# Optimization experiments

Hardware: AMD Instinct MI355X
Metric: run time of the kernel (lower is better)

The kernel has to match this reference:

```python
import jax, jax.numpy as jnp
import numpy as np

B, S, D = 2, 2048, 1280
H = 20
HD = D // H  # 64, rotary dim


def setup_inputs() -> dict:
    key = jax.random.key(0)
    ks = jax.random.split(key, 4)
    scale = 0.02
    return {
        "hidden_states": jax.random.normal(ks[0], (B, S, D), jnp.float32),
        "Wq": jax.random.normal(ks[1], (D, D), jnp.float32) * scale,
        "bq": jnp.zeros((D,), jnp.float32),
        "Wk": jax.random.normal(ks[2], (D, D), jnp.float32) * scale,
        "bk": jnp.zeros((D,), jnp.float32),
        "Wv": jax.random.normal(ks[3], (D, D), jnp.float32) * scale,
        "bv": jnp.zeros((D,), jnp.float32),
    }


def _rotate_half(x):
    x1, x2 = jnp.split(x, 2, axis=-1)
    return jnp.concatenate((-x2, x1), axis=-1)


def _rotary_cos_sin(seq_len, dim, dtype):
    inv_freq = 1.0 / (10000.0 ** (jnp.arange(0, dim, 2, dtype=jnp.float32) / dim))
    t = jnp.arange(seq_len, dtype=jnp.float32)
    freqs = jnp.einsum("i,j->ij", t, inv_freq)          # [S, dim/2]
    emb = jnp.concatenate((freqs, freqs), axis=-1)        # [S, dim]
    return jnp.cos(emb).astype(dtype)[None, None], jnp.sin(emb).astype(dtype)[None, None]


def reference(hidden_states, Wq, bq, Wk, bk, Wv, bv):
    b, s, d = hidden_states.shape
    # QKV projections, split heads -> [B, H, S, HD]
    def proj(W, bias):
        y = hidden_states @ W + bias
        return y.reshape(b, s, H, HD).transpose(0, 2, 1, 3)

    q = proj(Wq, bq) * (HD ** -0.5)  # scale BEFORE rotary, as in source
    k = proj(Wk, bk)
    v = proj(Wv, bv)

    cos, sin = _rotary_cos_sin(s, HD, q.dtype)
    q = q * cos + _rotate_half(q) * sin
    k = k * cos + _rotate_half(k) * sin

    scores = jnp.einsum("bhqd,bhkd->bhqk", q, k)
    probs = jax.nn.softmax(scores, axis=-1)
    ctx = jnp.einsum("bhqk,bhkd->bhqd", probs, v)
    return ctx.transpose(0, 2, 1, 3).reshape(b, s, d)
```

## Files before the change

### kernel.cpp

```cpp
#include <hip/hip_runtime.h>

#define DD 1280
#define SS 2048
#define HH 20

typedef __bf16 bf16x8 __attribute__((ext_vector_type(8)));
typedef float f32x4 __attribute__((ext_vector_type(4)));

typedef __attribute__((address_space(3))) unsigned int lds_uint;
typedef __attribute__((address_space(1))) unsigned int glb_uint;
#define GLL16(g, l) __builtin_amdgcn_global_load_lds((const glb_uint*)(g), (lds_uint*)(l), 16, 0, 0)

__device__ __forceinline__ unsigned short f2bf(float f) {
  union { float f; unsigned u; } v; v.f = f;
  unsigned r = v.u + 0x7fffu + ((v.u >> 16) & 1u);
  return (unsigned short)(r >> 16);
}
__device__ __forceinline__ unsigned f2u(float f) {
  union { float f; unsigned u; } v; v.f = f; return v.u;
}
__device__ __forceinline__ unsigned pk2(float lo, float hi) {
  return ((unsigned)f2bf(hi) << 16) | (unsigned)f2bf(lo);
}

__global__ __launch_bounds__(256) void prep_kernel(
    const float* __restrict__ X, const float* __restrict__ Wq,
    const float* __restrict__ Wk, const float* __restrict__ Wv,
    unsigned short* __restrict__ Xb, unsigned short* __restrict__ WT,
    float2* __restrict__ cs) {
  __shared__ __align__(8) unsigned short tile[32][36];
  int bid = blockIdx.x, tid = threadIdx.x;
  if (bid < 2560) {
    size_t base = (size_t)bid * 2048 + (size_t)tid * 8;
    const float4* xin = (const float4*)(X + base);
    float4 a = xin[0], c = xin[1];
    uint4 o = make_uint4(pk2(a.x, a.y), pk2(a.z, a.w), pk2(c.x, c.y), pk2(c.z, c.w));
    *(uint4*)(Xb + base) = o;
  } else if (bid < 7360) {
    int wb = bid - 2560;
    int mat = wb / 1600;
    int t = wb % 1600;
    int tn = t % 40, tk = t / 40;
    const float* W = (mat == 0) ? Wq : ((mat == 1) ? Wk : Wv);
    int k0 = tk * 32, n0 = tn * 32;
    int r = tid >> 3, cq = tid & 7;
    float4 wv = *(const float4*)(W + (size_t)(k0 + r) * DD + n0 + cq * 4);
    *(ushort4*)&tile[r][cq * 4] =
        make_ushort4(f2bf(wv.x), f2bf(wv.y), f2bf(wv.z), f2bf(wv.w));
    __syncthreads();
    unsigned short* out = WT + (size_t)mat * DD * DD;
    ushort4 o = make_ushort4(tile[cq * 4 + 0][r], tile[cq * 4 + 1][r],
                             tile[cq * 4 + 2][r], tile[cq * 4 + 3][r]);
    *(ushort4*)(out + (size_t)(n0 + r) * DD + k0 + cq * 4) = o;
  } else {
    int idx = (bid - 7360) * 256 + tid;
    int sp = idx >> 5, j = idx & 31;
    float invf = exp2f(-(float)j * 0.41524101186092034f);
    float ang = (float)sp * invf;
    cs[idx] = make_float2(cosf(ang), sinf(ang));
  }
}

__global__ __launch_bounds__(256) void qkv_gemm_kernel(
    const unsigned short* __restrict__ Xb, const unsigned short* __restrict__ WT,
    const float* __restrict__ bq, const float* __restrict__ bk, const float* __restrict__ bv,
    const float2* __restrict__ cs,
    unsigned short* __restrict__ Qr, unsigned short* __restrict__ Kr,
    unsigned short* __restrict__ VT) {
  __shared__ __align__(16) unsigned short As[128 * 32];
  __shared__ __align__(16) unsigned short Bs[128 * 32];
  int bx0 = blockIdx.x;
  int bx = (bx0 & 7) * 120 + (bx0 >> 3);
  int mat = bx / 320;
  int r0 = bx % 320;
  int tm = r0 / 10, tn = r0 % 10;
  int m0 = tm * 128, n0 = tn * 128;
  int tid = threadIdx.x;
  int lane = tid & 63, wave = tid >> 6;
  int c15 = lane & 15, quad = lane >> 4;
  int wm = wave >> 1, wn = wave & 1;
  const unsigned short* Wm = WT + (size_t)mat * DD * DD;

  int rowA = tid >> 2;
  int c8 = (tid & 3) * 8;
  const unsigned short* gA0 = Xb + (size_t)(m0 + rowA) * DD + c8;
  const unsigned short* gA1 = gA0 + (size_t)64 * DD;
  const unsigned short* gB0 = Wm + (size_t)(n0 + rowA) * DD + c8;
  const unsigned short* gB1 = gB0 + (size_t)64 * DD;
  unsigned short* ldsA0 = As + wave * 512;
  unsigned short* ldsA1 = As + 2048 + wave * 512;
  unsigned short* ldsB0 = Bs + wave * 512;
  unsigned short* ldsB1 = Bs + 2048 + wave * 512;

  f32x4 acc[4][4] = {};

  for (int kk = 0; kk < DD; kk += 32) {
    __syncthreads();
    GLL16(gA0 + kk, ldsA0);
    GLL16(gA1 + kk, ldsA1);
    GLL16(gB0 + kk, ldsB0);
    GLL16(gB1 + kk, ldsB1);
    __syncthreads();
    bf16x8 af[4];
#pragma unroll
    for (int mi = 0; mi < 4; mi++)
      af[mi] = *(const bf16x8*)(As + (wm * 64 + mi * 16 + c15) * 32 + quad * 8);
#pragma unroll
    for (int ni = 0; ni < 4; ni++) {
      bf16x8 bfr = *(const bf16x8*)(Bs + (wn * 64 + ni * 16 + c15) * 32 + quad * 8);
#pragma unroll
      for (int mi = 0; mi < 4; mi++)
        acc[mi][ni] = __builtin_amdgcn_mfma_f32_16x16x32_bf16(af[mi], bfr, acc[mi][ni], 0, 0, 0);
    }
  }

  int growb = m0 + wm * 64;
  int gcolb = n0 + wn * 64;
  if (mat == 2) {
#pragma unroll
    for (int mi = 0; mi < 4; mi++) {
      int row0 = growb + mi * 16 + quad * 4;
      int bb_ = row0 >> 11, sp = row0 & 2047;
#pragma unroll
      for (int ni = 0; ni < 4; ni++) {
        int gcol = gcolb + ni * 16 + c15;
        float bias = bv[gcol];
        int hh = gcol >> 6, dd = gcol & 63;
        f32x4 v = acc[mi][ni];
        ushort4 o = make_ushort4(f2bf(v[0] + bias), f2bf(v[1] + bias),
                                 f2bf(v[2] + bias), f2bf(v[3] + bias));
        *(ushort4*)(VT + ((size_t)((bb_ * HH + hh) * 64 + dd)) * SS + sp) = o;
      }
    }
  } else {
    unsigned short* Out = (mat == 0) ? Qr : Kr;
    const float* bias = (mat == 0) ? bq : bk;
    float qs = (mat == 0) ? 0.18033688011112042f : 1.0f;
#pragma unroll
    for (int mi = 0; mi < 4; mi++) {
      int row0 = growb + mi * 16 + quad * 4;
#pragma unroll
      for (int ni = 0; ni < 2; ni++) {
        int gcol_lo = gcolb + ni * 16 + c15;
        int gcol_hi = gcol_lo + 32;
        float blo = bias[gcol_lo], bhi = bias[gcol_hi];
        int d = ni * 16 + c15;
        f32x4 lo = acc[mi][ni], hi = acc[mi][ni + 2];
#pragma unroll
        for (int r = 0; r < 4; r++) {
          int grow = row0 + r;
          float2 cv = cs[(size_t)(grow & 2047) * 32 + d];
          float xl = (lo[r] + blo) * qs, xh = (hi[r] + bhi) * qs;
          Out[(size_t)grow * DD + gcol_lo] = f2bf(xl * cv.x - xh * cv.y);
          Out[(size_t)grow * DD + gcol_hi] = f2bf(xh * cv.x + xl * cv.y);
        }
      }
    }
  }
}

__device__ __forceinline__ void attn_load_frags(
    bf16x8 (&kf)[2][2], bf16x8 (&vf)[4],
    const unsigned short* Kt, const unsigned short* Vt, int c15, int quad) {
#pragma unroll
  for (int ni = 0; ni < 2; ni++)
#pragma unroll
    for (int kc = 0; kc < 2; kc++)
      kf[ni][kc] = *(const bf16x8*)(Kt + (size_t)(ni * 16 + c15) * DD + kc * 32 + quad * 8);
#pragma unroll
  for (int nio = 0; nio < 4; nio++)
    vf[nio] = *(const bf16x8*)(Vt + (size_t)(nio * 16 + c15) * SS + quad * 8);
}

__device__ __forceinline__ void attn_tile(
    const bf16x8 (&qf)[4][2], const bf16x8 (&kf)[2][2], const bf16x8 (&vf)[4],
    const bf16x8& ones, f32x4 (&of)[4][4], f32x4 (&ol)[4],
    unsigned short* Pw, int c15, int quad) {
  f32x4 sc[4][2] = {};
#pragma unroll
  for (int ni = 0; ni < 2; ni++)
#pragma unroll
    for (int kc = 0; kc < 2; kc++)
#pragma unroll
      for (int mi = 0; mi < 4; mi++)
        sc[mi][ni] = __builtin_amdgcn_mfma_f32_16x16x32_bf16(qf[mi][kc], kf[ni][kc], sc[mi][ni], 0, 0, 0);

  int pos_r = (quad + 2 * ((c15 >> 2) & 3) + (c15 & 3)) & 7;

#define PROD(mi)                                                              \
  {                                                                           \
    _Pragma("unroll")                                                         \
    for (int ni = 0; ni < 2; ni++) {                                          \
      int kc8 = ni * 2 + (c15 >> 3);                                          \
      _Pragma("unroll")                                                       \
      for (int r = 0; r < 4; r++) {                                           \
        unsigned u = f2u(__builtin_amdgcn_exp2f(sc[mi][ni][r]));              \
        int q = (mi) * 16 + quad * 4 + r;                                     \
        int pos = (kc8 + 2 * quad + r) & 7;                                   \
        Pw[q * 64 + pos * 8 + (c15 & 7)] = (unsigned short)(u >> 16);         \
      }                                                                       \
    }                                                                         \
  }
#define CONS(mi)                                                              \
  {                                                                           \
    bf16x8 pf = *(const bf16x8*)(Pw + ((mi) * 16 + c15) * 64 + pos_r * 8);    \
    _Pragma("unroll")                                                         \
    for (int nio = 0; nio < 4; nio++)                                         \
      of[mi][nio] = __builtin_amdgcn_mfma_f32_16x16x32_bf16(pf, vf[nio],      \
                                                            of[mi][nio], 0, 0, 0); \
    ol[mi] = __builtin_amdgcn_mfma_f32_16x16x32_bf16(pf, ones, ol[mi], 0, 0, 0); \
  }

  PROD(0);
  PROD(1); CONS(0);
  PROD(2); CONS(1);
  PROD(3); CONS(2);
  CONS(3);
#undef PROD
#undef CONS
}

__global__ __launch_bounds__(256)
__attribute__((amdgpu_waves_per_eu(2, 4)))
void attn_kernel(
    const unsigned short* __restrict__ Qr, const unsigned short* __restrict__ Kr,
    const unsigned short* __restrict__ VT, float* __restrict__ out) {
  __shared__ __align__(16) unsigned short Pall[4 * 64 * 64];
  __shared__ float Lbuf[64];
  int bx = blockIdx.x;
  int bh = bx % 40, qt = bx / 40;
  int b = bh / HH, h = bh % HH;
  int tid = threadIdx.x;
  int lane = tid & 63, w = tid >> 6;
  int c15 = lane & 15, quad = lane >> 4;
  int q0 = qt * 64;

  const unsigned short* Qbase = Qr + (size_t)(b * SS + q0) * DD + h * 64;
  bf16x8 qf[4][2];
#pragma unroll
  for (int mi = 0; mi < 4; mi++)
#pragma unroll
    for (int kc = 0; kc < 2; kc++)
      qf[mi][kc] = *(const bf16x8*)(Qbase + (size_t)(mi * 16 + c15) * DD + kc * 32 + quad * 8);

  const unsigned short* Kbase = Kr + (size_t)(b * SS + w * 32) * DD + h * 64;
  const unsigned short* Vbase = VT + (size_t)(bh * 64) * SS + w * 32;
  unsigned short* Pw = Pall + w * 4096;

  bf16x8 ones;
#pragma unroll
  for (int i = 0; i < 8; i++) ones[i] = (__bf16)1.0f;

  f32x4 of[4][4] = {};
  f32x4 ol[4] = {};

  bf16x8 kfb[2][2][2], vfb[2][4];
  attn_load_frags(kfb[0], vfb[0], Kbase, Vbase, c15, quad);

  for (int t = 0; t < 16; t += 2) {
    attn_load_frags(kfb[1], vfb[1],
                    Kbase + (size_t)((t + 1) * 128) * DD, Vbase + (t + 1) * 128,
                    c15, quad);
    attn_tile(qf, kfb[0], vfb[0], ones, of, ol, Pw, c15, quad);
    if (t + 2 < 16)
      attn_load_frags(kfb[0], vfb[0],
                      Kbase + (size_t)((t + 2) * 128) * DD, Vbase + (t + 2) * 128,
                      c15, quad);
    attn_tile(qf, kfb[1], vfb[1], ones, of, ol, Pw, c15, quad);
  }

  __syncthreads();
  float* Obuf = (float*)Pall;

  for (int pass = 0; pass < 4; pass++) {
    if (w == pass) {
#pragma unroll
      for (int mi = 0; mi < 4; mi++)
#pragma unroll
        for (int nio = 0; nio < 4; nio++)
#pragma unroll
          for (int r = 0; r < 4; r++) {
            int q = mi * 16 + quad * 4 + r;
            int d = nio * 16 + c15;
            if (pass == 0) Obuf[q * 65 + d] = of[mi][nio][r];
            else           Obuf[q * 65 + d] += of[mi][nio][r];
          }
      if (c15 == 0) {
#pragma unroll
        for (int mi = 0; mi < 4; mi++)
#pragma unroll
          for (int r = 0; r < 4; r++) {
            int q = mi * 16 + quad * 4 + r;
            if (pass == 0) Lbuf[q] = ol[mi][r];
            else           Lbuf[q] += ol[mi][r];
          }
      }
    }
    __syncthreads();
  }

  {
    int row = w * 16 + (lane >> 2);
    int col0 = (lane & 3) * 16;
    float invl = 1.0f / Lbuf[row];
    float* op = out + (size_t)(b * SS + q0 + row) * DD + h * 64 + col0;
    const float* ob = Obuf + row * 65 + col0;
#pragma unroll
    for (int j = 0; j < 4; j++) {
      float4 v = make_float4(ob[j * 4 + 0] * invl, ob[j * 4 + 1] * invl,
                             ob[j * 4 + 2] * invl, ob[j * 4 + 3] * invl);
      *(float4*)(op + j * 4) = v;
    }
  }
}

extern "C" void kernel_launch(void* const* d_in, const int* in_sizes, int n_in,
                              void* d_out, int out_size, void* d_ws, size_t ws_size,
                              hipStream_t stream) {
  (void)in_sizes; (void)n_in; (void)out_size; (void)ws_size;
  const float* X  = (const float*)d_in[0];
  const float* Wq = (const float*)d_in[1];
  const float* bq = (const float*)d_in[2];
  const float* Wk = (const float*)d_in[3];
  const float* bk = (const float*)d_in[4];
  const float* Wv = (const float*)d_in[5];
  const float* bv = (const float*)d_in[6];
  char* ws = (char*)d_ws;
  unsigned short* Xb  = (unsigned short*)(ws);
  unsigned short* WT  = (unsigned short*)(ws + 10485760);
  unsigned short* Qr  = (unsigned short*)(ws + 20316160);
  unsigned short* Kr  = (unsigned short*)(ws + 30801920);
  unsigned short* VTt = (unsigned short*)(ws + 41287680);
  float2* cstab       = (float2*)(ws + 51773440);
  hipLaunchKernelGGL(prep_kernel, dim3(7616), dim3(256), 0, stream, X, Wq, Wk, Wv, Xb, WT, cstab);
  hipLaunchKernelGGL(qkv_gemm_kernel, dim3(960), dim3(256), 0, stream, Xb, WT, bq, bk, bv, cstab, Qr, Kr, VTt);
  hipLaunchKernelGGL(attn_kernel, dim3(1280), dim3(256), 0, stream, Qr, Kr, VTt, (float*)d_out);
}
```

Baseline: 242.2 us.

## Restructure attention to split queries across waves with shared LDS K/V tiles

The attention kernel now gives each wave its own 16 query rows instead of having all four waves split the key range over the same 64 queries. K and V tiles of 32 keys are staged once per block into double-buffered, XOR-swizzled LDS with global_load_lds, and all waves share them. This removes the cross-wave reduction of partial outputs and row sums through LDS at the end, and cuts register use. The cost is a block-wide barrier on every one of the 64 key steps and smaller MFMA work per step, which may expose latency. The waves_per_eu attribute is also dropped.

New measurement: 234.0 us. 1.04x faster.

```diff
diff --git a/kernel.cpp b/kernel.cpp
--- a/kernel.cpp
+++ b/kernel.cpp
@@ -159,158 +159,93 @@
   }
 }
 
-__device__ __forceinline__ void attn_load_frags(
-    bf16x8 (&kf)[2][2], bf16x8 (&vf)[4],
-    const unsigned short* Kt, const unsigned short* Vt, int c15, int quad) {
-#pragma unroll
-  for (int ni = 0; ni < 2; ni++)
-#pragma unroll
-    for (int kc = 0; kc < 2; kc++)
-      kf[ni][kc] = *(const bf16x8*)(Kt + (size_t)(ni * 16 + c15) * DD + kc * 32 + quad * 8);
-#pragma unroll
-  for (int nio = 0; nio < 4; nio++)
-    vf[nio] = *(const bf16x8*)(Vt + (size_t)(nio * 16 + c15) * SS + quad * 8);
-}
-
-__device__ __forceinline__ void attn_tile(
-    const bf16x8 (&qf)[4][2], const bf16x8 (&kf)[2][2], const bf16x8 (&vf)[4],
-    const bf16x8& ones, f32x4 (&of)[4][4], f32x4 (&ol)[4],
-    unsigned short* Pw, int c15, int quad) {
-  f32x4 sc[4][2] = {};
-#pragma unroll
-  for (int ni = 0; ni < 2; ni++)
-#pragma unroll
-    for (int kc = 0; kc < 2; kc++)
-#pragma unroll
-      for (int mi = 0; mi < 4; mi++)
-        sc[mi][ni] = __builtin_amdgcn_mfma_f32_16x16x32_bf16(qf[mi][kc], kf[ni][kc], sc[mi][ni], 0, 0, 0);
-
-  int pos_r = (quad + 2 * ((c15 >> 2) & 3) + (c15 & 3)) & 7;
-
-#define PROD(mi)                                                              \
-  {                                                                           \
-    _Pragma("unroll")                                                         \
-    for (int ni = 0; ni < 2; ni++) {                                          \
-      int kc8 = ni * 2 + (c15 >> 3);                                          \
-      _Pragma("unroll")                                                       \
-      for (int r = 0; r < 4; r++) {                                           \
-        unsigned u = f2u(__builtin_amdgcn_exp2f(sc[mi][ni][r]));              \
-        int q = (mi) * 16 + quad * 4 + r;                                     \
-        int pos = (kc8 + 2 * quad + r) & 7;                                   \
-        Pw[q * 64 + pos * 8 + (c15 & 7)] = (unsigned short)(u >> 16);         \
-      }                                                                       \
-    }                                                                         \
-  }
-#define CONS(mi)                                                              \
-  {                                                                           \
-    bf16x8 pf = *(const bf16x8*)(Pw + ((mi) * 16 + c15) * 64 + pos_r * 8);    \
-    _Pragma("unroll")                                                         \
-    for (int nio = 0; nio < 4; nio++)                                         \
-      of[mi][nio] = __builtin_amdgcn_mfma_f32_16x16x32_bf16(pf, vf[nio],      \
-                                                            of[mi][nio], 0, 0, 0); \
-    ol[mi] = __builtin_amdgcn_mfma_f32_16x16x32_bf16(pf, ones, ol[mi], 0, 0, 0); \
-  }
-
-  PROD(0);
-  PROD(1); CONS(0);
-  PROD(2); CONS(1);
-  PROD(3); CONS(2);
-  CONS(3);
-#undef PROD
-#undef CONS
-}
-
 __global__ __launch_bounds__(256)
-__attribute__((amdgpu_waves_per_eu(2, 4)))
 void attn_kernel(
     const unsigned short* __restrict__ Qr, const unsigned short* __restrict__ Kr,
     const unsigned short* __restrict__ VT, float* __restrict__ out) {
-  __shared__ __align__(16) unsigned short Pall[4 * 64 * 64];
-  __shared__ float Lbuf[64];
+  __shared__ __align__(16) unsigned short Klds[2][2048];
+  __shared__ __align__(16) unsigned short Vlds[2][2048];
+  __shared__ __align__(16) unsigned short Pall[4][512];
   int bx = blockIdx.x;
   int bh = bx % 40, qt = bx / 40;
   int b = bh / HH, h = bh % HH;
   int tid = threadIdx.x;
   int lane = tid & 63, w = tid >> 6;
   int c15 = lane & 15, quad = lane >> 4;
-  int q0 = qt * 64;
-
-  const unsigned short* Qbase = Qr + (size_t)(b * SS + q0) * DD + h * 64;
-  bf16x8 qf[4][2];
-#pragma unroll
-  for (int mi = 0; mi < 4; mi++)
+  int q0 = qt * 64 + w * 16;
+
+  const unsigned short* Qb = Qr + (size_t)(b * SS + q0 + c15) * DD + h * 64 + quad * 8;
+  bf16x8 qf[2];
+  qf[0] = *(const bf16x8*)(Qb);
+  qf[1] = *(const bf16x8*)(Qb + 32);
+
+  int krow = tid >> 3, kch = tid & 7;
+  const unsigned short* Ksrc = Kr + (size_t)(b * SS + krow) * DD + h * 64
+                               + ((kch ^ (krow & 7)) * 8);
+  int vrow = tid >> 2, vch = tid & 3;
+  const unsigned short* Vsrc = VT + (size_t)(bh * 64 + vrow) * SS
+                               + ((vch ^ ((vrow >> 1) & 3)) * 8);
+  unsigned short* Pw = &Pall[w][0];
+
+  bf16x8 ones;
+#pragma unroll
+  for (int i = 0; i < 8; i++) ones[i] = (__bf16)1.0f;
+
+  f32x4 of[4] = {};
+  f32x4 ol = {};
+
+  GLL16(Ksrc, &Klds[0][0] + w * 512);
+  GLL16(Vsrc, &Vlds[0][0] + w * 512);
+  __syncthreads();
+
+  for (int t = 0; t < 64; t++) {
+    int buf = t & 1;
+    if (t + 1 < 64) {
+      GLL16(Ksrc + (size_t)((t + 1) * 32) * DD, &Klds[buf ^ 1][0] + w * 512);
+      GLL16(Vsrc + (t + 1) * 32, &Vlds[buf ^ 1][0] + w * 512);
+    }
+    const unsigned short* Kb = &Klds[buf][0];
+    const unsigned short* Vb = &Vlds[buf][0];
+
+    f32x4 sc[2] = {};
 #pragma unroll
     for (int kc = 0; kc < 2; kc++)
-      qf[mi][kc] = *(const bf16x8*)(Qbase + (size_t)(mi * 16 + c15) * DD + kc * 32 + quad * 8);
-
-  const unsigned short* Kbase = Kr + (size_t)(b * SS + w * 32) * DD + h * 64;
-  const unsigned short* Vbase = VT + (size_t)(bh * 64) * SS + w * 32;
-  unsigned short* Pw = Pall + w * 4096;
-
-  bf16x8 ones;
-#pragma unroll
-  for (int i = 0; i < 8; i++) ones[i] = (__bf16)1.0f;
-
-  f32x4 of[4][4] = {};
-  f32x4 ol[4] = {};
-
-  bf16x8 kfb[2][2][2], vfb[2][4];
-  attn_load_frags(kfb[0], vfb[0], Kbase, Vbase, c15, quad);
-
-  for (int t = 0; t < 16; t += 2) {
-    attn_load_frags(kfb[1], vfb[1],
-                    Kbase + (size_t)((t + 1) * 128) * DD, Vbase + (t + 1) * 128,
-                    c15, quad);
-    attn_tile(qf, kfb[0], vfb[0], ones, of, ol, Pw, c15, quad);
-    if (t + 2 < 16)
-      attn_load_frags(kfb[0], vfb[0],
-                      Kbase + (size_t)((t + 2) * 128) * DD, Vbase + (t + 2) * 128,
-                      c15, quad);
-    attn_tile(qf, kfb[1], vfb[1], ones, of, ol, Pw, c15, quad);
-  }
-
-  __syncthreads();
-  float* Obuf = (float*)Pall;
-
-  for (int pass = 0; pass < 4; pass++) {
-    if (w == pass) {
-#pragma unroll
-      for (int mi = 0; mi < 4; mi++)
-#pragma unroll
-        for (int nio = 0; nio < 4; nio++)
-#pragma unroll
-          for (int r = 0; r < 4; r++) {
-            int q = mi * 16 + quad * 4 + r;
-            int d = nio * 16 + c15;
-            if (pass == 0) Obuf[q * 65 + d] = of[mi][nio][r];
-            else           Obuf[q * 65 + d] += of[mi][nio][r];
-          }
-      if (c15 == 0) {
-#pragma unroll
-        for (int mi = 0; mi < 4; mi++)
-#pragma unroll
-          for (int r = 0; r < 4; r++) {
-            int q = mi * 16 + quad * 4 + r;
-            if (pass == 0) Lbuf[q] = ol[mi][r];
-            else           Lbuf[q] += ol[mi][r];
-          }
-      }
-    }
-    __syncthreads();
-  }
-
-  {
-    int row = w * 16 + (lane >> 2);
-    int col0 = (lane & 3) * 16;
-    float invl = 1.0f / Lbuf[row];
-    float* op = out + (size_t)(b * SS + q0 + row) * DD + h * 64 + col0;
-    const float* ob = Obuf + row * 65 + col0;
-#pragma unroll
-    for (int j = 0; j < 4; j++) {
-      float4 v = make_float4(ob[j * 4 + 0] * invl, ob[j * 4 + 1] * invl,
-                             ob[j * 4 + 2] * invl, ob[j * 4 + 3] * invl);
-      *(float4*)(op + j * 4) = v;
-    }
+#pragma unroll
+      for (int ni = 0; ni < 2; ni++) {
+        int R = ni * 16 + c15;
+        bf16x8 kf = *(const bf16x8*)(Kb + R * 64 + (((kc * 4 + quad) ^ (R & 7)) * 8));
+        sc[ni] = __builtin_amdgcn_mfma_f32_16x16x32_bf16(qf[kc], kf, sc[ni], 0, 0, 0);
+      }
+
+#pragma unroll
+    for (int ni = 0; ni < 2; ni++)
+#pragma unroll
+      for (int r = 0; r < 4; r++) {
+        unsigned u = f2u(__builtin_amdgcn_exp2f(sc[ni][r]));
+        int q = quad * 4 + r;
+        int sw = (ni * 2 + (c15 >> 3)) ^ ((q >> 1) & 3);
+        Pw[q * 32 + sw * 8 + (c15 & 7)] = (unsigned short)(u >> 16);
+      }
+
+    bf16x8 pf = *(const bf16x8*)(Pw + c15 * 32 + ((quad ^ ((c15 >> 1) & 3)) * 8));
+#pragma unroll
+    for (int nio = 0; nio < 4; nio++) {
+      int R = nio * 16 + c15;
+      bf16x8 vf = *(const bf16x8*)(Vb + R * 32 + ((quad ^ ((R >> 1) & 3)) * 8));
+      of[nio] = __builtin_amdgcn_mfma_f32_16x16x32_bf16(pf, vf, of[nio], 0, 0, 0);
+    }
+    ol = __builtin_amdgcn_mfma_f32_16x16x32_bf16(pf, ones, ol, 0, 0, 0);
+
+    __syncthreads();
+  }
+
+#pragma unroll
+  for (int r = 0; r < 4; r++) {
+    float invl = 1.0f / ol[r];
+    float* op = out + (size_t)(b * SS + q0 + quad * 4 + r) * DD + h * 64 + c15;
+#pragma unroll
+    for (int nio = 0; nio < 4; nio++)
+      op[nio * 16] = of[nio][r] * invl;
   }
 }
 
```
